# Kernel optimization log

Measured on AMD Instinct MI355X. Metric: run time of the kernel, lower is better.

Reference implementation:

```python
import jax, jax.numpy as jnp
import numpy as np

V, C, COUT, DEG = 50000, 128, 256, 16
E = V * DEG


def setup_inputs() -> dict:
    key = jax.random.key(0)
    k1, k2, k3, k4 = jax.random.split(key, 4)
    data = jax.random.normal(k1, (V, C), dtype=jnp.float32)
    # Every vertex gets exactly DEG neighbors -> sorted segment ids.
    edge_src = jnp.repeat(jnp.arange(V, dtype=jnp.int32), DEG)
    edge_dst = jax.random.randint(k2, (E,), 0, V, dtype=jnp.int32)
    # Row-normalized neighbor weights (sum over each vertex's edges == 1).
    raw_w = jax.random.uniform(k3, (E,), dtype=jnp.float32) + 0.1
    row_sum = jax.ops.segment_sum(raw_w, edge_src, num_segments=V)
    edge_w = raw_w / row_sum[edge_src]
    kernel = jax.random.normal(k4, (2 * C, COUT), dtype=jnp.float32) * (1.0 / np.sqrt(2 * C))
    bias = jnp.zeros((COUT,), dtype=jnp.float32)
    return {"data": data, "edge_src": edge_src, "edge_dst": edge_dst,
            "edge_w": edge_w, "kernel": kernel, "bias": bias}


def reference(data, edge_src, edge_dst, edge_w, kernel, bias):
    # Gather per-edge endpoint features: x = data[i], y = data[j].
    x = data[edge_src]                       # [E, C]
    y = data[edge_dst]                       # [E, C]
    # Edge function h(x, y) = Linear([x, y - x]) (1x1 Conv1D, no activation).
    feat = jnp.concatenate([x, y - x], axis=-1)          # [E, 2C]
    edge_out = feat @ kernel + bias                       # [E, COUT]
    # reduction='weighted': out[i] = sum_j w_ij * h(x_i, x_j).
    out = jax.ops.segment_sum(edge_w[:, None] * edge_out, edge_src,
                              num_segments=data.shape[0])  # [V, COUT]
    return out
```

## Files before the change

### kernel.cpp

```cpp
#include <hip/hip_runtime.h>
#include <hip/hip_bf16.h>
#include <cstdint>

#define V_N    50000
#define C_N    128
#define COUT_N 256
#define DEG_N  16
#define K2_N   256

typedef short bf16x8 __attribute__((ext_vector_type(8)));
typedef float f32x4  __attribute__((ext_vector_type(4)));
typedef float f32x2  __attribute__((ext_vector_type(2)));

__device__ __forceinline__ unsigned short f2bf(float f) {
    union { float f; unsigned u; } a; a.f = f;
    unsigned r = a.u + 0x7fffu + ((a.u >> 16) & 1u);
    return (unsigned short)(r >> 16);
}

__global__ __launch_bounds__(256)
void prep_kernel(const float* __restrict__ data, const float* __restrict__ kern,
                 unsigned* __restrict__ db8, unsigned short* __restrict__ bt) {
    const int b = blockIdx.x;
    if (b < 3125) {
        const int i = b * 256 + threadIdx.x;
        const float4 f0 = *reinterpret_cast<const float4*>(data + (size_t)i * 8);
        const float4 f1 = *reinterpret_cast<const float4*>(data + (size_t)i * 8 + 4);
        unsigned lo = 0, hi = 0;
        lo = __builtin_amdgcn_cvt_pk_fp8_f32(f0.x, f0.y, lo, false);
        lo = __builtin_amdgcn_cvt_pk_fp8_f32(f0.z, f0.w, lo, true);
        hi = __builtin_amdgcn_cvt_pk_fp8_f32(f1.x, f1.y, hi, false);
        hi = __builtin_amdgcn_cvt_pk_fp8_f32(f1.z, f1.w, hi, true);
        uint2 o; o.x = lo; o.y = hi;
        *reinterpret_cast<uint2*>(db8 + (size_t)i * 2) = o;
    } else {
        const int k = b - 3125;
        const int n = threadIdx.x;
        const int idx = (((n >> 4) * 8 + (k >> 5)) * 4 + ((k >> 3) & 3)) * 128
                      + (n & 15) * 8 + (k & 7);
        bt[idx] = f2bf(kern[k * COUT_N + n]);
    }
}

__global__ __launch_bounds__(512, 4)
void dgc_fused_kernel(const float* __restrict__ data,
                      const unsigned char* __restrict__ db8,
                      const int* __restrict__ edge_dst,
                      const float* __restrict__ edge_w,
                      const unsigned short* __restrict__ btg,
                      const float* __restrict__ bias,
                      float* __restrict__ out) {
    __shared__ __align__(16) char Asm[32 * 512];

    const int tid  = threadIdx.x;
    const int lane = tid & 63;
    const int wid  = __builtin_amdgcn_readfirstlane(tid >> 6);
    const int m0   = blockIdx.x * 32;
    const int g    = lane >> 4;
    const int c    = lane & 15;

    const int row = wid * 4 + g;
    const int cv  = min(m0 + row, V_N - 1);

    const uint4*  ed4 = reinterpret_cast<const uint4*>(edge_dst + (size_t)cv * DEG_N);
    const float4* ew4 = reinterpret_cast<const float4*>(edge_w  + (size_t)cv * DEG_N);

    const float4 xa = *reinterpret_cast<const float4*>(data + (size_t)cv * C_N + c * 8);
    const float4 xb = *reinterpret_cast<const float4*>(data + (size_t)cv * C_N + c * 8 + 4);

    float s[8];
    #pragma unroll
    for (int i = 0; i < 8; ++i) s[i] = 0.f;
    float Ws = 0.f;

    #pragma unroll
    for (int half = 0; half < 2; ++half) {
        const uint4  jq0 = ed4[half * 2 + 0];
        const uint4  jq1 = ed4[half * 2 + 1];
        const float4 wq0 = ew4[half * 2 + 0];
        const float4 wq1 = ew4[half * 2 + 1];
        const unsigned jj[8] = { jq0.x, jq0.y, jq0.z, jq0.w,
                                 jq1.x, jq1.y, jq1.z, jq1.w };
        const float    ww[8] = { wq0.x, wq0.y, wq0.z, wq0.w,
                                 wq1.x, wq1.y, wq1.z, wq1.w };

        uint2 h[8];
        #pragma unroll
        for (int e = 0; e < 8; ++e)
            h[e] = *reinterpret_cast<const uint2*>(
                db8 + (size_t)jj[e] * C_N + c * 8);
        __builtin_amdgcn_sched_barrier(0);

        #pragma unroll
        for (int e = 0; e < 8; ++e) {
            const f32x2 p0 = __builtin_amdgcn_cvt_pk_f32_fp8(h[e].x, false);
            const f32x2 p1 = __builtin_amdgcn_cvt_pk_f32_fp8(h[e].x, true);
            const f32x2 p2 = __builtin_amdgcn_cvt_pk_f32_fp8(h[e].y, false);
            const f32x2 p3 = __builtin_amdgcn_cvt_pk_f32_fp8(h[e].y, true);
            const float wk = ww[e];
            s[0] = fmaf(wk, p0[0], s[0]);
            s[1] = fmaf(wk, p0[1], s[1]);
            s[2] = fmaf(wk, p1[0], s[2]);
            s[3] = fmaf(wk, p1[1], s[3]);
            s[4] = fmaf(wk, p2[0], s[4]);
            s[5] = fmaf(wk, p2[1], s[5]);
            s[6] = fmaf(wk, p3[0], s[6]);
            s[7] = fmaf(wk, p3[1], s[7]);
        }
        Ws += ((ww[0] + ww[1]) + (ww[2] + ww[3]))
            + ((ww[4] + ww[5]) + (ww[6] + ww[7]));
    }

    {
        float u[8], v[8];
        u[0] = Ws * xa.x; u[1] = Ws * xa.y; u[2] = Ws * xa.z; u[3] = Ws * xa.w;
        u[4] = Ws * xb.x; u[5] = Ws * xb.y; u[6] = Ws * xb.z; u[7] = Ws * xb.w;
        #pragma unroll
        for (int i = 0; i < 8; ++i) v[i] = s[i] - u[i];
        uint4 up, vp;
        up.x = (unsigned)f2bf(u[0]) | ((unsigned)f2bf(u[1]) << 16);
        up.y = (unsigned)f2bf(u[2]) | ((unsigned)f2bf(u[3]) << 16);
        up.z = (unsigned)f2bf(u[4]) | ((unsigned)f2bf(u[5]) << 16);
        up.w = (unsigned)f2bf(u[6]) | ((unsigned)f2bf(u[7]) << 16);
        vp.x = (unsigned)f2bf(v[0]) | ((unsigned)f2bf(v[1]) << 16);
        vp.y = (unsigned)f2bf(v[2]) | ((unsigned)f2bf(v[3]) << 16);
        vp.z = (unsigned)f2bf(v[4]) | ((unsigned)f2bf(v[5]) << 16);
        vp.w = (unsigned)f2bf(v[6]) | ((unsigned)f2bf(v[7]) << 16);
        const int sw = row & 7;
        char* rowp = Asm + row * 512;
        *reinterpret_cast<uint4*>(rowp + ((c        ^ sw) * 16)) = up;
        *reinterpret_cast<uint4*>(rowp + (((16 + c) ^ sw) * 16)) = vp;
    }
    __syncthreads();

    const int wm = wid >> 2;
    const int wn = wid & 3;

    f32x4 acc[4];
    #pragma unroll
    for (int nf = 0; nf < 4; ++nf)
        acc[nf] = (f32x4){0.f, 0.f, 0.f, 0.f};

    #pragma unroll
    for (int ks = 0; ks < 8; ++ks) {
        bf16x8 a, b[4];
        {
            const int r  = wm * 16 + c;
            const int ck = (ks * 4 + g) ^ (r & 7);
            a = *reinterpret_cast<const bf16x8*>(Asm + r * 512 + ck * 16);
        }
        #pragma unroll
        for (int nf = 0; nf < 4; ++nf) {
            const int nb = wn * 4 + nf;
            b[nf] = *reinterpret_cast<const bf16x8*>(
                btg + (size_t)((nb * 32 + ks * 4 + g) * 16 + c) * 8);
        }
        #pragma unroll
        for (int nf = 0; nf < 4; ++nf)
            acc[nf] = __builtin_amdgcn_mfma_f32_16x16x32_bf16(a, b[nf], acc[nf], 0, 0, 0);
    }

    {
        const int row_l = wm * 16 + g * 4;
        #pragma unroll
        for (int nf = 0; nf < 4; ++nf) {
            const int col = wn * 64 + nf * 16 + c;
            const float bb = bias[col];
            #pragma unroll
            for (int r = 0; r < 4; ++r) {
                const int rg = m0 + row_l + r;
                if (rg < V_N)
                    out[(size_t)rg * COUT_N + col] = acc[nf][r] + bb;
            }
        }
    }
}

extern "C" void kernel_launch(void* const* d_in, const int* in_sizes, int n_in,
                              void* d_out, int out_size, void* d_ws, size_t ws_size,
                              hipStream_t stream) {
    const float* data     = (const float*)d_in[0];
    const int*   edge_dst = (const int*)d_in[2];
    const float* edge_w   = (const float*)d_in[3];
    const float* kern     = (const float*)d_in[4];
    const float* bias     = (const float*)d_in[5];
    float*       out      = (float*)d_out;

    unsigned short* bt  = (unsigned short*)d_ws;
    unsigned char*  db8 = (unsigned char*)d_ws + 131072;

    prep_kernel<<<3125 + 256, 256, 0, stream>>>(data, kern, (unsigned*)db8, bt);

    const int nblk = (V_N + 31) / 32;
    dgc_fused_kernel<<<nblk, 512, 0, stream>>>(data, db8, edge_dst, edge_w, bt, bias, out);
}
```

Baseline: 134.8 us.

## Halve block to 256 threads with wider per-lane gathers and 2x4 MFMA tiles

Each 32-row block now uses 4 waves instead of 8. In the gather phase each lane loads 16 fp8 bytes per neighbor (uint4) instead of 8, and the 16 edges are processed in a single streamed loop with no sched barrier. In the GEMM phase each wave computes all 32 rows for its 64 columns, reusing each B fragment across two M fragments. This cuts B global loads per block and widens memory transactions, at the cost of more registers per thread and less latency hiding from having fewer waves.

```diff
diff --git a/kernel.cpp b/kernel.cpp
--- a/kernel.cpp
+++ b/kernel.cpp
@@ -42,7 +42,7 @@
     }
 }
 
-__global__ __launch_bounds__(512, 4)
+__global__ __launch_bounds__(256, 4)
 void dgc_fused_kernel(const float* __restrict__ data,
                       const unsigned char* __restrict__ db8,
                       const int* __restrict__ edge_dst,
@@ -56,98 +56,111 @@
     const int lane = tid & 63;
     const int wid  = __builtin_amdgcn_readfirstlane(tid >> 6);
     const int m0   = blockIdx.x * 32;
-    const int g    = lane >> 4;
-    const int c    = lane & 15;
-
-    const int row = wid * 4 + g;
+
+    const int g8 = lane >> 3;
+    const int c8 = lane & 7;
+
+    const int row = wid * 8 + g8;
     const int cv  = min(m0 + row, V_N - 1);
 
     const uint4*  ed4 = reinterpret_cast<const uint4*>(edge_dst + (size_t)cv * DEG_N);
     const float4* ew4 = reinterpret_cast<const float4*>(edge_w  + (size_t)cv * DEG_N);
 
-    const float4 xa = *reinterpret_cast<const float4*>(data + (size_t)cv * C_N + c * 8);
-    const float4 xb = *reinterpret_cast<const float4*>(data + (size_t)cv * C_N + c * 8 + 4);
-
-    float s[8];
-    #pragma unroll
-    for (int i = 0; i < 8; ++i) s[i] = 0.f;
+    const float4* xp = reinterpret_cast<const float4*>(data + (size_t)cv * C_N + c8 * 16);
+    const float4 x0 = xp[0], x1 = xp[1], x2 = xp[2], x3 = xp[3];
+
+    float s[16];
+    #pragma unroll
+    for (int i = 0; i < 16; ++i) s[i] = 0.f;
     float Ws = 0.f;
 
-    #pragma unroll
-    for (int half = 0; half < 2; ++half) {
-        const uint4  jq0 = ed4[half * 2 + 0];
-        const uint4  jq1 = ed4[half * 2 + 1];
-        const float4 wq0 = ew4[half * 2 + 0];
-        const float4 wq1 = ew4[half * 2 + 1];
-        const unsigned jj[8] = { jq0.x, jq0.y, jq0.z, jq0.w,
-                                 jq1.x, jq1.y, jq1.z, jq1.w };
-        const float    ww[8] = { wq0.x, wq0.y, wq0.z, wq0.w,
-                                 wq1.x, wq1.y, wq1.z, wq1.w };
-
-        uint2 h[8];
-        #pragma unroll
-        for (int e = 0; e < 8; ++e)
-            h[e] = *reinterpret_cast<const uint2*>(
-                db8 + (size_t)jj[e] * C_N + c * 8);
-        __builtin_amdgcn_sched_barrier(0);
-
-        #pragma unroll
-        for (int e = 0; e < 8; ++e) {
-            const f32x2 p0 = __builtin_amdgcn_cvt_pk_f32_fp8(h[e].x, false);
-            const f32x2 p1 = __builtin_amdgcn_cvt_pk_f32_fp8(h[e].x, true);
-            const f32x2 p2 = __builtin_amdgcn_cvt_pk_f32_fp8(h[e].y, false);
-            const f32x2 p3 = __builtin_amdgcn_cvt_pk_f32_fp8(h[e].y, true);
-            const float wk = ww[e];
-            s[0] = fmaf(wk, p0[0], s[0]);
-            s[1] = fmaf(wk, p0[1], s[1]);
-            s[2] = fmaf(wk, p1[0], s[2]);
-            s[3] = fmaf(wk, p1[1], s[3]);
-            s[4] = fmaf(wk, p2[0], s[4]);
-            s[5] = fmaf(wk, p2[1], s[5]);
-            s[6] = fmaf(wk, p3[0], s[6]);
-            s[7] = fmaf(wk, p3[1], s[7]);
-        }
-        Ws += ((ww[0] + ww[1]) + (ww[2] + ww[3]))
-            + ((ww[4] + ww[5]) + (ww[6] + ww[7]));
-    }
+#define GATH(J, WK)                                                           \
+    do {                                                                      \
+        const uint4 h = *reinterpret_cast<const uint4*>(                      \
+            db8 + (size_t)(J) * C_N + c8 * 16);                               \
+        const f32x2 p0 = __builtin_amdgcn_cvt_pk_f32_fp8(h.x, false);         \
+        const f32x2 p1 = __builtin_amdgcn_cvt_pk_f32_fp8(h.x, true);          \
+        const f32x2 p2 = __builtin_amdgcn_cvt_pk_f32_fp8(h.y, false);         \
+        const f32x2 p3 = __builtin_amdgcn_cvt_pk_f32_fp8(h.y, true);          \
+        const f32x2 p4 = __builtin_amdgcn_cvt_pk_f32_fp8(h.z, false);         \
+        const f32x2 p5 = __builtin_amdgcn_cvt_pk_f32_fp8(h.z, true);          \
+        const f32x2 p6 = __builtin_amdgcn_cvt_pk_f32_fp8(h.w, false);         \
+        const f32x2 p7 = __builtin_amdgcn_cvt_pk_f32_fp8(h.w, true);          \
+        s[ 0] = fmaf((WK), p0[0], s[ 0]);  s[ 1] = fmaf((WK), p0[1], s[ 1]);  \
+        s[ 2] = fmaf((WK), p1[0], s[ 2]);  s[ 3] = fmaf((WK), p1[1], s[ 3]);  \
+        s[ 4] = fmaf((WK), p2[0], s[ 4]);  s[ 5] = fmaf((WK), p2[1], s[ 5]);  \
+        s[ 6] = fmaf((WK), p3[0], s[ 6]);  s[ 7] = fmaf((WK), p3[1], s[ 7]);  \
+        s[ 8] = fmaf((WK), p4[0], s[ 8]);  s[ 9] = fmaf((WK), p4[1], s[ 9]);  \
+        s[10] = fmaf((WK), p5[0], s[10]);  s[11] = fmaf((WK), p5[1], s[11]);  \
+        s[12] = fmaf((WK), p6[0], s[12]);  s[13] = fmaf((WK), p6[1], s[13]);  \
+        s[14] = fmaf((WK), p7[0], s[14]);  s[15] = fmaf((WK), p7[1], s[15]);  \
+    } while (0)
+
+    #pragma unroll
+    for (int kq = 0; kq < 4; ++kq) {
+        const uint4  jq = ed4[kq];
+        const float4 wq = ew4[kq];
+        GATH(jq.x, wq.x);
+        GATH(jq.y, wq.y);
+        GATH(jq.z, wq.z);
+        GATH(jq.w, wq.w);
+        Ws += (wq.x + wq.y) + (wq.z + wq.w);
+    }
+#undef GATH
 
     {
-        float u[8], v[8];
-        u[0] = Ws * xa.x; u[1] = Ws * xa.y; u[2] = Ws * xa.z; u[3] = Ws * xa.w;
-        u[4] = Ws * xb.x; u[5] = Ws * xb.y; u[6] = Ws * xb.z; u[7] = Ws * xb.w;
-        #pragma unroll
-        for (int i = 0; i < 8; ++i) v[i] = s[i] - u[i];
-        uint4 up, vp;
-        up.x = (unsigned)f2bf(u[0]) | ((unsigned)f2bf(u[1]) << 16);
-        up.y = (unsigned)f2bf(u[2]) | ((unsigned)f2bf(u[3]) << 16);
-        up.z = (unsigned)f2bf(u[4]) | ((unsigned)f2bf(u[5]) << 16);
-        up.w = (unsigned)f2bf(u[6]) | ((unsigned)f2bf(u[7]) << 16);
-        vp.x = (unsigned)f2bf(v[0]) | ((unsigned)f2bf(v[1]) << 16);
-        vp.y = (unsigned)f2bf(v[2]) | ((unsigned)f2bf(v[3]) << 16);
-        vp.z = (unsigned)f2bf(v[4]) | ((unsigned)f2bf(v[5]) << 16);
-        vp.w = (unsigned)f2bf(v[6]) | ((unsigned)f2bf(v[7]) << 16);
+        float u[16], v[16];
+        u[ 0] = Ws * x0.x; u[ 1] = Ws * x0.y; u[ 2] = Ws * x0.z; u[ 3] = Ws * x0.w;
+        u[ 4] = Ws * x1.x; u[ 5] = Ws * x1.y; u[ 6] = Ws * x1.z; u[ 7] = Ws * x1.w;
+        u[ 8] = Ws * x2.x; u[ 9] = Ws * x2.y; u[10] = Ws * x2.z; u[11] = Ws * x2.w;
+        u[12] = Ws * x3.x; u[13] = Ws * x3.y; u[14] = Ws * x3.z; u[15] = Ws * x3.w;
+        #pragma unroll
+        for (int i = 0; i < 16; ++i) v[i] = s[i] - u[i];
+        uint4 up0, up1, vp0, vp1;
+        up0.x = (unsigned)f2bf(u[ 0]) | ((unsigned)f2bf(u[ 1]) << 16);
+        up0.y = (unsigned)f2bf(u[ 2]) | ((unsigned)f2bf(u[ 3]) << 16);
+        up0.z = (unsigned)f2bf(u[ 4]) | ((unsigned)f2bf(u[ 5]) << 16);
+        up0.w = (unsigned)f2bf(u[ 6]) | ((unsigned)f2bf(u[ 7]) << 16);
+        up1.x = (unsigned)f2bf(u[ 8]) | ((unsigned)f2bf(u[ 9]) << 16);
+        up1.y = (unsigned)f2bf(u[10]) | ((unsigned)f2bf(u[11]) << 16);
+        up1.z = (unsigned)f2bf(u[12]) | ((unsigned)f2bf(u[13]) << 16);
+        up1.w = (unsigned)f2bf(u[14]) | ((unsigned)f2bf(u[15]) << 16);
+        vp0.x = (unsigned)f2bf(v[ 0]) | ((unsigned)f2bf(v[ 1]) << 16);
+        vp0.y = (unsigned)f2bf(v[ 2]) | ((unsigned)f2bf(v[ 3]) << 16);
+        vp0.z = (unsigned)f2bf(v[ 4]) | ((unsigned)f2bf(v[ 5]) << 16);
+        vp0.w = (unsigned)f2bf(v[ 6]) | ((unsigned)f2bf(v[ 7]) << 16);
+        vp1.x = (unsigned)f2bf(v[ 8]) | ((unsigned)f2bf(v[ 9]) << 16);
+        vp1.y = (unsigned)f2bf(v[10]) | ((unsigned)f2bf(v[11]) << 16);
+        vp1.z = (unsigned)f2bf(v[12]) | ((unsigned)f2bf(v[13]) << 16);
+        vp1.w = (unsigned)f2bf(v[14]) | ((unsigned)f2bf(v[15]) << 16);
         const int sw = row & 7;
         char* rowp = Asm + row * 512;
-        *reinterpret_cast<uint4*>(rowp + ((c        ^ sw) * 16)) = up;
-        *reinterpret_cast<uint4*>(rowp + (((16 + c) ^ sw) * 16)) = vp;
+        *reinterpret_cast<uint4*>(rowp + (((2 * c8 + 0)      ^ sw) * 16)) = up0;
+        *reinterpret_cast<uint4*>(rowp + (((2 * c8 + 1)      ^ sw) * 16)) = up1;
+        *reinterpret_cast<uint4*>(rowp + (((16 + 2 * c8 + 0) ^ sw) * 16)) = vp0;
+        *reinterpret_cast<uint4*>(rowp + (((16 + 2 * c8 + 1) ^ sw) * 16)) = vp1;
     }
     __syncthreads();
 
-    const int wm = wid >> 2;
-    const int wn = wid & 3;
-
-    f32x4 acc[4];
-    #pragma unroll
-    for (int nf = 0; nf < 4; ++nf)
-        acc[nf] = (f32x4){0.f, 0.f, 0.f, 0.f};
+    const int g  = lane >> 4;
+    const int c  = lane & 15;
+    const int wn = wid;
+
+    f32x4 acc[2][4];
+    #pragma unroll
+    for (int mf = 0; mf < 2; ++mf)
+        #pragma unroll
+        for (int nf = 0; nf < 4; ++nf)
+            acc[mf][nf] = (f32x4){0.f, 0.f, 0.f, 0.f};
 
     #pragma unroll
     for (int ks = 0; ks < 8; ++ks) {
-        bf16x8 a, b[4];
-        {
-            const int r  = wm * 16 + c;
+        bf16x8 a[2], b[4];
+        #pragma unroll
+        for (int mf = 0; mf < 2; ++mf) {
+            const int r  = mf * 16 + c;
             const int ck = (ks * 4 + g) ^ (r & 7);
-            a = *reinterpret_cast<const bf16x8*>(Asm + r * 512 + ck * 16);
+            a[mf] = *reinterpret_cast<const bf16x8*>(Asm + r * 512 + ck * 16);
         }
         #pragma unroll
         for (int nf = 0; nf < 4; ++nf) {
@@ -156,12 +169,16 @@
                 btg + (size_t)((nb * 32 + ks * 4 + g) * 16 + c) * 8);
         }
         #pragma unroll
-        for (int nf = 0; nf < 4; ++nf)
-            acc[nf] = __builtin_amdgcn_mfma_f32_16x16x32_bf16(a, b[nf], acc[nf], 0, 0, 0);
-    }
-
-    {
-        const int row_l = wm * 16 + g * 4;
+        for (int mf = 0; mf < 2; ++mf)
+            #pragma unroll
+            for (int nf = 0; nf < 4; ++nf)
+                acc[mf][nf] = __builtin_amdgcn_mfma_f32_16x16x32_bf16(
+                    a[mf], b[nf], acc[mf][nf], 0, 0, 0);
+    }
+
+    #pragma unroll
+    for (int mf = 0; mf < 2; ++mf) {
+        const int row_l = mf * 16 + g * 4;
         #pragma unroll
         for (int nf = 0; nf < 4; ++nf) {
             const int col = wn * 64 + nf * 16 + c;
@@ -170,7 +187,7 @@
             for (int r = 0; r < 4; ++r) {
                 const int rg = m0 + row_l + r;
                 if (rg < V_N)
-                    out[(size_t)rg * COUT_N + col] = acc[nf][r] + bb;
+                    out[(size_t)rg * COUT_N + col] = acc[mf][nf][r] + bb;
             }
         }
     }
@@ -192,5 +209,5 @@
     prep_kernel<<<3125 + 256, 256, 0, stream>>>(data, kern, (unsigned*)db8, bt);
 
     const int nblk = (V_N + 31) / 32;
-    dgc_fused_kernel<<<nblk, 512, 0, stream>>>(data, db8, edge_dst, edge_w, bt, bias, out);
-}
+    dgc_fused_kernel<<<nblk, 256, 0, stream>>>(data, db8, edge_dst, edge_w, bt, bias, out);
+}
```

Result: faster. 127.4 us (-5.5%).
